# Optimization experiments

Measured on AMD Instinct MI355X. Metric: run time of the kernel, lower is better.

Reference implementation:

```python
import jax, jax.numpy as jnp
import numpy as np

DIM = 128          # per-head dim P (== feature dim of x, y)
HEADS = 8
INNER = DIM * HEADS  # 1024
HIDDEN = int(DIM * 4.0)  # 512
EPS = 1e-5
LS_INIT = 1e-5


def _ln(x, w, b):
    mu = jnp.mean(x, axis=-1, keepdims=True)
    var = jnp.var(x, axis=-1, keepdims=True)
    return (x - mu) * jax.lax.rsqrt(var + EPS) * w + b


def setup_inputs() -> dict:
    key = jax.random.key(0)
    ks = jax.random.split(key, 10)
    B, N, M = 8, 1024, 1024
    s_in = 1.0 / np.sqrt(DIM)
    s_inner = 1.0 / np.sqrt(INNER)
    s_hid = 1.0 / np.sqrt(HIDDEN)
    return {
        "x": jax.random.normal(ks[0], (B, N, DIM), jnp.float32),
        "y": jax.random.normal(ks[1], (B, M, DIM), jnp.float32),
        "norm_x_w": jnp.ones((DIM,), jnp.float32),
        "norm_x_b": jnp.zeros((DIM,), jnp.float32),
        "norm_y_w": jnp.ones((DIM,), jnp.float32),
        "norm_y_b": jnp.zeros((DIM,), jnp.float32),
        "q_w": jax.random.uniform(ks[2], (INNER, DIM), jnp.float32, -s_in, s_in),
        "kv_w": jax.random.uniform(ks[3], (2 * INNER, DIM), jnp.float32, -s_in, s_in),
        "proj_w": jax.random.uniform(ks[4], (DIM, INNER), jnp.float32, -s_inner, s_inner),
        "proj_b": jax.random.uniform(ks[5], (DIM,), jnp.float32, -s_inner, s_inner),
        "ls1_gamma": jnp.full((DIM,), LS_INIT, jnp.float32),
        "norm_out_w": jnp.ones((DIM,), jnp.float32),
        "norm_out_b": jnp.zeros((DIM,), jnp.float32),
        "fc1_w": jax.random.uniform(ks[6], (HIDDEN, DIM), jnp.float32, -s_in, s_in),
        "fc1_b": jax.random.uniform(ks[7], (HIDDEN,), jnp.float32, -s_in, s_in),
        "fc2_w": jax.random.uniform(ks[8], (DIM, HIDDEN), jnp.float32, -s_hid, s_hid),
        "fc2_b": jax.random.uniform(ks[9], (DIM,), jnp.float32, -s_hid, s_hid),
        "ls2_gamma": jnp.full((DIM,), LS_INIT, jnp.float32),
    }


def reference(x, y, norm_x_w, norm_x_b, norm_y_w, norm_y_b, q_w, kv_w,
              proj_w, proj_b, ls1_gamma, norm_out_w, norm_out_b,
              fc1_w, fc1_b, fc2_w, fc2_b, ls2_gamma):
    B, N, P = x.shape
    M = y.shape[1]
    scale = P ** (-0.5)

    xn = _ln(x, norm_x_w, norm_x_b)
    yn = _ln(y, norm_y_w, norm_y_b)

    # q: (B,N,H,P) -> bhnp ; kv: (B,M,2,H,P)
    q = (xn @ q_w.T).reshape(B, N, HEADS, P).transpose(0, 2, 1, 3)
    kv = (yn @ kv_w.T).reshape(B, M, 2, HEADS, P)
    k = kv[:, :, 0].transpose(0, 2, 1, 3)  # bhmp
    v = kv[:, :, 1].transpose(0, 2, 1, 3)  # bhmp

    attn = jnp.einsum('bhnp,bhmp->bhnm', q, k) * scale
    attn = jax.nn.softmax(attn, axis=-1)
    o = jnp.einsum('bhnm,bhmp->bhnp', attn, v)
    o = o.transpose(0, 2, 1, 3).reshape(B, N, INNER)
    o = o @ proj_w.T + proj_b
    x = x + o * ls1_gamma

    h = _ln(x, norm_out_w, norm_out_b)
    h = jax.nn.relu(h @ fc1_w.T + fc1_b)
    h = h @ fc2_w.T + fc2_b
    x = x + h * ls2_gamma
    return x
```

## Files before the change

### kernel.cpp

```cpp
#include <hip/hip_runtime.h>
#include <stdint.h>

#define DIM    128
#define HEADS  8
#define INNER  1024
#define HIDDEN 512
#define BATCH  8
#define SEQ    1024
#define ROWS   8192

typedef __attribute__((ext_vector_type(8))) short bf16x8;
typedef __attribute__((ext_vector_type(4))) float f32x4;
typedef __attribute__((ext_vector_type(4))) unsigned short u16x4;

#define QSCALE (0.08838834764831845f * 1.4426950408889634f)

#define AS1 __attribute__((address_space(1)))
#define AS3 __attribute__((address_space(3)))

static __device__ __forceinline__ float b2f(unsigned short u) {
    union { float f; unsigned int i; } v; v.i = ((unsigned int)u) << 16; return v.f;
}
static __device__ __forceinline__ unsigned short f2b(float f) {
    union { float f; unsigned int i; } v; v.f = f;
    unsigned int x = v.i;
    return (unsigned short)((x + 0x7fffu + ((x >> 16) & 1u)) >> 16);
}
static __device__ __forceinline__ unsigned int cvt_pk_bf16(float a, float b) {
    unsigned int r;
    asm("v_cvt_pk_bf16_f32 %0, %1, %2" : "=v"(r) : "v"(a), "v"(b));
    return r;
}
static __device__ __forceinline__ void gl_lds16(const unsigned short* g, unsigned short* l) {
    __builtin_amdgcn_global_load_lds((AS1 void*)g, (AS3 void*)l, 16, 0, 0);
}

static __device__ __forceinline__ size_t pa_idx(int row, int k, int K) {
    return ((size_t)((row >> 4) * (K >> 5) + (k >> 5)) << 9)
         + (size_t)(((((k >> 3) & 3) << 4) + (row & 15)) << 3) + (size_t)(k & 7);
}

template<int K>
static __device__ __forceinline__ void cvtw(const float* __restrict__ W,
                                            unsigned short* __restrict__ Wp, int j)
{
    const int c  = j & 15;
    const int gw = (j >> 4) & 3;
    const int blk = j >> 6;
    const int ks = blk & ((K >> 5) - 1);
    const int nt = blk / (K >> 5);
    const int n  = nt * 16 + c;
    const int kb = ks * 32 + gw * 8;
    const float4 a = *(const float4*)(W + (size_t)n * K + kb);
    const float4 b = *(const float4*)(W + (size_t)n * K + kb + 4);
    u16x4 o0, o1;
    o0[0] = f2b(a.x); o0[1] = f2b(a.y); o0[2] = f2b(a.z); o0[3] = f2b(a.w);
    o1[0] = f2b(b.x); o1[1] = f2b(b.y); o1[2] = f2b(b.z); o1[3] = f2b(b.w);
    *(u16x4*)(Wp + (size_t)j * 8)     = o0;
    *(u16x4*)(Wp + (size_t)j * 8 + 4) = o1;
}

__global__ __launch_bounds__(256)
void cvt_all_kernel(const float* __restrict__ s0, unsigned short* __restrict__ d0,
                    const float* __restrict__ s1, unsigned short* __restrict__ d1,
                    const float* __restrict__ s2, unsigned short* __restrict__ d2,
                    const float* __restrict__ s3, unsigned short* __restrict__ d3,
                    const float* __restrict__ s4, unsigned short* __restrict__ d4)
{
    int j = blockIdx.x * 256 + threadIdx.x;
    if (j < 16384)                 { cvtw<128>(s0, d0, j);  return; }
    if ((j -= 16384) < 32768)      { cvtw<128>(s1, d1, j);  return; }
    if ((j -= 32768) < 16384)      { cvtw<1024>(s2, d2, j); return; }
    if ((j -= 16384) < 8192)       { cvtw<128>(s3, d3, j);  return; }
    j -= 8192;                       cvtw<512>(s4, d4, j);
}

static __device__ __forceinline__ void ln_row(const float* __restrict__ in,
                                              const float* __restrict__ w,
                                              const float* __restrict__ b,
                                              unsigned short* __restrict__ out,
                                              int row, int lane)
{
    const float2 xv = *(const float2*)(in + (size_t)row*DIM + lane*2);
    float x0 = xv.x, x1 = xv.y;
    float s = x0 + x1;
    float q = x0*x0 + x1*x1;
    #pragma unroll
    for (int off = 32; off > 0; off >>= 1) {
        s += __shfl_xor(s, off);
        q += __shfl_xor(q, off);
    }
    const float mu  = s * (1.0f/128.0f);
    const float var = q * (1.0f/128.0f) - mu*mu;
    const float rs  = rsqrtf(var + 1e-5f);
    const float2 wv = *(const float2*)(w + lane*2);
    const float2 bv = *(const float2*)(b + lane*2);
    unsigned short o0 = f2b((x0 - mu) * rs * wv.x + bv.x);
    unsigned short o1 = f2b((x1 - mu) * rs * wv.y + bv.y);
    *(unsigned int*)(out + pa_idx(row, lane*2, 128)) = (unsigned int)o0 | ((unsigned int)o1 << 16);
}

__global__ __launch_bounds__(256)
void ln_dual_kernel(const float* __restrict__ inx, const float* __restrict__ wx,
                    const float* __restrict__ bx, unsigned short* __restrict__ outx,
                    const float* __restrict__ iny, const float* __restrict__ wy,
                    const float* __restrict__ by, unsigned short* __restrict__ outy)
{
    const int row  = blockIdx.x * 4 + (threadIdx.x >> 6);
    const int lane = threadIdx.x & 63;
    if (blockIdx.y == 0) ln_row(inx, wx, bx, outx, row, lane);
    else                 ln_row(iny, wy, by, outy, row, lane);
}

__global__ __launch_bounds__(256)
void qkv_kernel(const unsigned short* __restrict__ xn,
                const unsigned short* __restrict__ yn,
                const unsigned short* __restrict__ wq,
                const unsigned short* __restrict__ wkv,
                unsigned short* __restrict__ qb,
                unsigned short* __restrict__ kpm,
                unsigned short* __restrict__ vpm)
{
    const int lane = threadIdx.x & 63;
    const int wave = threadIdx.x >> 6;
    const int g    = lane >> 4;
    const int c16  = lane & 15;
    const int bx   = blockIdx.x;
    const bool isq = bx < 16;
    const unsigned short* A = isq ? xn : yn;
    const unsigned short* W = isq ? wq : wkv;
    const int nt0  = (isq ? bx : bx - 16) * 4;
    const int mb   = blockIdx.y * 64 + wave * 16;
    const int nb   = nt0 * 16;
    const int mt   = blockIdx.y * 4 + wave;

    f32x4 acc[4];
    #pragma unroll
    for (int t = 0; t < 4; ++t) acc[t] = (f32x4){0.f, 0.f, 0.f, 0.f};

    #pragma unroll
    for (int ks = 0; ks < 4; ++ks) {
        bf16x8 af = *(const bf16x8*)(A + (((size_t)(mt*4 + ks)) << 9) + lane*8);
        #pragma unroll
        for (int t = 0; t < 4; ++t) {
            bf16x8 wf = *(const bf16x8*)(W + (((size_t)((nt0 + t)*4 + ks)) << 9) + lane*8);
            acc[t] = __builtin_amdgcn_mfma_f32_16x16x32_bf16(af, wf, acc[t], 0, 0, 0);
        }
    }

    #pragma unroll
    for (int t = 0; t < 4; ++t) {
        #pragma unroll
        for (int r = 0; r < 4; ++r) {
            const int row = mb + g*4 + r;
            const int col = nb + t*16 + c16;
            const float v = acc[t][r];
            const int bb = row >> 10, m = row & 1023;
            if (isq) {
                const int hh = col >> 7, p = col & 127;
                qb[(((size_t)(bb*HEADS + hh))*SEQ + m)*DIM + p] = f2b(v * QSCALE);
            } else {
                const int chunk = m >> 5;
                if (col < INNER) {
                    const int hh = col >> 7, p = col & 127;
                    const int sl = (m >> 4) & 1, cl = m & 15;
                    const int ksl = p >> 5, gl = (p >> 3) & 3, el = p & 7;
                    kpm[(size_t)(bb*HEADS + hh)*SEQ*DIM
                        + (size_t)((chunk*8 + sl*4 + ksl)*64 + gl*16 + cl)*8 + el] = f2b(v);
                } else {
                    const int c2 = col - INNER;
                    const int hh = c2 >> 7, p = c2 & 127;
                    const int gl = (m >> 3) & 3, el = m & 7;
                    const int pcl = p >> 4, cl = p & 15;
                    vpm[(size_t)(bb*HEADS + hh)*SEQ*DIM
                        + (size_t)((chunk*8 + pcl)*64 + gl*16 + cl)*8 + el] = f2b(v);
                }
            }
        }
    }
}

__global__ __launch_bounds__(512)
void attn_kernel(const unsigned short* __restrict__ qbuf,
                 const unsigned short* __restrict__ kperm,
                 const unsigned short* __restrict__ vperm,
                 unsigned short* __restrict__ obuf)
{
    __shared__ unsigned short kbuf[2][4096];
    __shared__ unsigned short vbuf[2][4096];
    __shared__ unsigned short pls[8][640];

    const int lane = threadIdx.x & 63;
    const int wave = threadIdx.x >> 6;
    const int g    = lane >> 4;
    const int c16  = lane & 15;

    const int j    = blockIdx.x;
    const int bh   = (j & 7) * 8 + (j >> 6);
    const int nblk = (j >> 3) & 7;
    const int n0   = nblk * 128 + wave * 16;
    const int bb   = bh >> 3, hh = bh & 7;

    const unsigned short* Q  = qbuf  + (size_t)bh * SEQ * DIM;
    const unsigned short* Kb = kperm + (size_t)bh * SEQ * DIM;
    const unsigned short* Vb = vperm + (size_t)bh * SEQ * DIM;

    gl_lds16(Kb + wave*512 + lane*8, &kbuf[0][wave*512]);
    gl_lds16(Vb + wave*512 + lane*8, &vbuf[0][wave*512]);

    bf16x8 qf[4];
    #pragma unroll
    for (int ks = 0; ks < 4; ++ks)
        qf[ks] = *(const bf16x8*)(Q + (size_t)(n0 + c16)*DIM + ks*32 + g*8);

    f32x4 oacc[8];
    #pragma unroll
    for (int pc = 0; pc < 8; ++pc) oacc[pc] = (f32x4){0.f,0.f,0.f,0.f};
    float mi = 8.0f;
    float li0 = 0.f, li1 = 0.f;

    __syncthreads();

    int cur = 0;
    for (int it = 0; it < 32; ++it, cur ^= 1) {
        if (it != 31) {
            const unsigned short* Ks = Kb + (size_t)(it + 1) * 4096;
            const unsigned short* Vs = Vb + (size_t)(it + 1) * 4096;
            gl_lds16(Ks + wave*512 + lane*8, &kbuf[cur ^ 1][wave*512]);
            gl_lds16(Vs + wave*512 + lane*8, &vbuf[cur ^ 1][wave*512]);
        }

        bf16x8 kf[2][4];
        #pragma unroll
        for (int s = 0; s < 2; ++s)
            #pragma unroll
            for (int ks = 0; ks < 4; ++ks)
                kf[s][ks] = *(const bf16x8*)&kbuf[cur][(s*4 + ks)*512 + lane*8];

        f32x4 st[2];
        #pragma unroll
        for (int s = 0; s < 2; ++s) {
            f32x4 a = (f32x4){0.f,0.f,0.f,0.f};
            #pragma unroll
            for (int ks = 0; ks < 4; ++ks)
                a = __builtin_amdgcn_mfma_f32_16x16x32_bf16(kf[s][ks], qf[ks], a, 0, 0, 0);
            st[s] = a;
        }

        bf16x8 vf[8];
        #pragma unroll
        for (int pc = 0; pc < 8; ++pc)
            vf[pc] = *(const bf16x8*)&vbuf[cur][(pc*64 + lane)*8];

        float cmax = st[0][0];
        cmax = fmaxf(cmax, st[0][1]); cmax = fmaxf(cmax, st[0][2]); cmax = fmaxf(cmax, st[0][3]);
        cmax = fmaxf(cmax, st[1][0]); cmax = fmaxf(cmax, st[1][1]);
        cmax = fmaxf(cmax, st[1][2]); cmax = fmaxf(cmax, st[1][3]);

        if (!__all(cmax - mi <= 8.0f)) {
            float rmax = cmax;
            rmax = fmaxf(rmax, __shfl_xor(rmax, 16));
            rmax = fmaxf(rmax, __shfl_xor(rmax, 32));
            const float mnew  = fmaxf(mi, rmax);
            const float alpha = exp2f(mi - mnew);
            mi = mnew;
            li0 *= alpha; li1 *= alpha;
            float ar[4];
            #pragma unroll
            for (int r = 0; r < 4; ++r) ar[r] = __shfl(alpha, g*4 + r);
            #pragma unroll
            for (int pc = 0; pc < 8; ++pc)
                #pragma unroll
                for (int r = 0; r < 4; ++r) oacc[pc][r] *= ar[r];
        }

        uint2 pw[2];
        {
            float p0 = exp2f(st[0][0] - mi), p1 = exp2f(st[0][1] - mi);
            float p2 = exp2f(st[0][2] - mi), p3 = exp2f(st[0][3] - mi);
            float p4 = exp2f(st[1][0] - mi), p5 = exp2f(st[1][1] - mi);
            float p6 = exp2f(st[1][2] - mi), p7 = exp2f(st[1][3] - mi);
            li0 += (p0 + p1) + (p2 + p3);
            li1 += (p4 + p5) + (p6 + p7);
            pw[0].x = cvt_pk_bf16(p0, p1); pw[0].y = cvt_pk_bf16(p2, p3);
            pw[1].x = cvt_pk_bf16(p4, p5); pw[1].y = cvt_pk_bf16(p6, p7);
        }

        unsigned short* pbase = &pls[wave][0];
        *(uint2*)(pbase + c16*40 + 0*16 + g*4) = pw[0];
        *(uint2*)(pbase + c16*40 + 1*16 + g*4) = pw[1];

        bf16x8 pa = *(const bf16x8*)(pbase + c16*40 + g*8);
        #pragma unroll
        for (int pc = 0; pc < 8; ++pc)
            oacc[pc] = __builtin_amdgcn_mfma_f32_16x16x32_bf16(pa, vf[pc], oacc[pc], 0, 0, 0);

        __syncthreads();
    }

    float li = li0 + li1;
    li += __shfl_xor(li, 16);
    li += __shfl_xor(li, 32);
    float lr[4];
    #pragma unroll
    for (int r = 0; r < 4; ++r) lr[r] = 1.f / __shfl(li, g*4 + r);
    #pragma unroll
    for (int pc = 0; pc < 8; ++pc)
        #pragma unroll
        for (int r = 0; r < 4; ++r) {
            const int row = bb*SEQ + n0 + g*4 + r;
            const int k   = hh*DIM + pc*16 + c16;
            obuf[pa_idx(row, k, INNER)] = f2b(oacc[pc][r] * lr[r]);
        }
}

__global__ __launch_bounds__(256)
void projln_kernel(const unsigned short* __restrict__ A,
                   const unsigned short* __restrict__ W,
                   const float* __restrict__ bias,
                   const float* __restrict__ gamma,
                   const float* __restrict__ xres,
                   float* __restrict__ x1,
                   const float* __restrict__ lnw, const float* __restrict__ lnb,
                   unsigned short* __restrict__ hin)
{
    __shared__ float part[4][16][2];

    const int lane = threadIdx.x & 63;
    const int wave = threadIdx.x >> 6;
    const int g    = lane >> 4;
    const int c16  = lane & 15;
    const int mt   = blockIdx.x;

    f32x4 acc[2];
    acc[0] = (f32x4){0.f,0.f,0.f,0.f};
    acc[1] = (f32x4){0.f,0.f,0.f,0.f};

    #pragma unroll 4
    for (int ks = 0; ks < 32; ++ks) {
        bf16x8 af = *(const bf16x8*)(A + (((size_t)(mt*32 + ks)) << 9) + lane*8);
        #pragma unroll
        for (int t = 0; t < 2; ++t) {
            bf16x8 wf = *(const bf16x8*)(W + (((size_t)((wave*2 + t)*32 + ks)) << 9) + lane*8);
            acc[t] = __builtin_amdgcn_mfma_f32_16x16x32_bf16(af, wf, acc[t], 0, 0, 0);
        }
    }

    float v[2][4];
    #pragma unroll
    for (int t = 0; t < 2; ++t) {
        const int col = wave*32 + t*16 + c16;
        const float bb = bias[col], gg = gamma[col];
        #pragma unroll
        for (int r = 0; r < 4; ++r) {
            const int row = mt*16 + g*4 + r;
            const float xv = xres[(size_t)row*DIM + col];
            v[t][r] = xv + (acc[t][r] + bb) * gg;
            x1[(size_t)row*DIM + col] = v[t][r];
        }
    }
    #pragma unroll
    for (int r = 0; r < 4; ++r) {
        float s = v[0][r] + v[1][r];
        float q = v[0][r]*v[0][r] + v[1][r]*v[1][r];
        #pragma unroll
        for (int off = 1; off < 16; off <<= 1) {
            s += __shfl_xor(s, off);
            q += __shfl_xor(q, off);
        }
        if (c16 == 0) { part[wave][g*4+r][0] = s; part[wave][g*4+r][1] = q; }
    }
    __syncthreads();

    #pragma unroll
    for (int r = 0; r < 4; ++r) {
        const int lr = g*4 + r;
        const float s = part[0][lr][0] + part[1][lr][0] + part[2][lr][0] + part[3][lr][0];
        const float q = part[0][lr][1] + part[1][lr][1] + part[2][lr][1] + part[3][lr][1];
        const float mu  = s * (1.0f/128.0f);
        const float var = q * (1.0f/128.0f) - mu*mu;
        const float rs  = rsqrtf(var + 1e-5f);
        const int row = mt*16 + lr;
        #pragma unroll
        for (int t = 0; t < 2; ++t) {
            const int col = wave*32 + t*16 + c16;
            const float hv = (v[t][r] - mu) * rs * lnw[col] + lnb[col];
            hin[pa_idx(row, col, 128)] = f2b(hv);
        }
    }
}

__global__ __launch_bounds__(256)
void fc_kernel(const unsigned short* __restrict__ hin,
               const unsigned short* __restrict__ W1,
               const float* __restrict__ b1,
               const unsigned short* __restrict__ W2,
               const float* __restrict__ b2,
               const float* __restrict__ gamma2,
               const float* __restrict__ x1,
               float* __restrict__ dout)
{
    __shared__ unsigned short h[16][520];

    const int lane = threadIdx.x & 63;
    const int wave = threadIdx.x >> 6;
    const int g    = lane >> 4;
    const int c16  = lane & 15;
    const int mt   = blockIdx.x;

    f32x4 a1[8];
    #pragma unroll
    for (int t = 0; t < 8; ++t) a1[t] = (f32x4){0.f,0.f,0.f,0.f};
    #pragma unroll
    for (int ks = 0; ks < 4; ++ks) {
        bf16x8 af = *(const bf16x8*)(hin + (((size_t)(mt*4 + ks)) << 9) + lane*8);
        #pragma unroll
        for (int t = 0; t < 8; ++t) {
            const int nt = wave*8 + t;
            bf16x8 wf = *(const bf16x8*)(W1 + (((size_t)(nt*4 + ks)) << 9) + lane*8);
            a1[t] = __builtin_amdgcn_mfma_f32_16x16x32_bf16(af, wf, a1[t], 0, 0, 0);
        }
    }
    #pragma unroll
    for (int t = 0; t < 8; ++t) {
        const int col = wave*128 + t*16 + c16;
        const float bb = b1[col];
        #pragma unroll
        for (int r = 0; r < 4; ++r)
            h[g*4 + r][col] = f2b(fmaxf(a1[t][r] + bb, 0.f));
    }
    __syncthreads();

    f32x4 a2[2];
    a2[0] = (f32x4){0.f,0.f,0.f,0.f};
    a2[1] = (f32x4){0.f,0.f,0.f,0.f};
    #pragma unroll 4
    for (int ks = 0; ks < 16; ++ks) {
        bf16x8 af = *(const bf16x8*)&h[c16][ks*32 + g*8];
        #pragma unroll
        for (int t = 0; t < 2; ++t) {
            const int nt = wave*2 + t;
            bf16x8 wf = *(const bf16x8*)(W2 + (((size_t)(nt*16 + ks)) << 9) + lane*8);
            a2[t] = __builtin_amdgcn_mfma_f32_16x16x32_bf16(af, wf, a2[t], 0, 0, 0);
        }
    }
    #pragma unroll
    for (int t = 0; t < 2; ++t) {
        const int col = wave*32 + t*16 + c16;
        const float bb = b2[col], gg = gamma2[col];
        #pragma unroll
        for (int r = 0; r < 4; ++r) {
            const int row = mt*16 + g*4 + r;
            dout[(size_t)row*DIM + col] = x1[(size_t)row*DIM + col] + (a2[t][r] + bb) * gg;
        }
    }
}

extern "C" void kernel_launch(void* const* d_in, const int* in_sizes, int n_in,
                              void* d_out, int out_size, void* d_ws, size_t ws_size,
                              hipStream_t stream)
{
    const float* x         = (const float*)d_in[0];
    const float* y         = (const float*)d_in[1];
    const float* norm_x_w  = (const float*)d_in[2];
    const float* norm_x_b  = (const float*)d_in[3];
    const float* norm_y_w  = (const float*)d_in[4];
    const float* norm_y_b  = (const float*)d_in[5];
    const float* q_w       = (const float*)d_in[6];
    const float* kv_w      = (const float*)d_in[7];
    const float* proj_w    = (const float*)d_in[8];
    const float* proj_b    = (const float*)d_in[9];
    const float* ls1_gamma = (const float*)d_in[10];
    const float* norm_o_w  = (const float*)d_in[11];
    const float* norm_o_b  = (const float*)d_in[12];
    const float* fc1_w     = (const float*)d_in[13];
    const float* fc1_b     = (const float*)d_in[14];
    const float* fc2_w     = (const float*)d_in[15];
    const float* fc2_b     = (const float*)d_in[16];
    const float* ls2_gamma = (const float*)d_in[17];

    char* ws = (char*)d_ws;
    size_t off = 0;
    auto alloc = [&](size_t bytes) {
        void* p = ws + off;
        off += (bytes + 255) & ~(size_t)255;
        return p;
    };
    unsigned short* xn  = (unsigned short*)alloc((size_t)ROWS*DIM*2);
    unsigned short* yn  = (unsigned short*)alloc((size_t)ROWS*DIM*2);
    unsigned short* qb  = (unsigned short*)alloc((size_t)ROWS*INNER*2);
    unsigned short* kpm = (unsigned short*)alloc((size_t)ROWS*INNER*2);
    unsigned short* vpm = (unsigned short*)alloc((size_t)ROWS*INNER*2);
    unsigned short* ob  = (unsigned short*)alloc((size_t)ROWS*INNER*2);
    float*          x1  = (float*)alloc((size_t)ROWS*DIM*4);
    unsigned short* hin = (unsigned short*)alloc((size_t)ROWS*DIM*2);
    unsigned short* wq   = (unsigned short*)alloc((size_t)INNER*DIM*2);
    unsigned short* wkv  = (unsigned short*)alloc((size_t)2*INNER*DIM*2);
    unsigned short* wpr  = (unsigned short*)alloc((size_t)DIM*INNER*2);
    unsigned short* wf1  = (unsigned short*)alloc((size_t)HIDDEN*DIM*2);
    unsigned short* wf2  = (unsigned short*)alloc((size_t)DIM*HIDDEN*2);

    cvt_all_kernel<<<dim3(320), 256, 0, stream>>>(
        q_w, wq, kv_w, wkv, proj_w, wpr, fc1_w, wf1, fc2_w, wf2);

    ln_dual_kernel<<<dim3(ROWS/4, 2), 256, 0, stream>>>(
        x, norm_x_w, norm_x_b, xn, y, norm_y_w, norm_y_b, yn);

    qkv_kernel<<<dim3(48, ROWS/64), 256, 0, stream>>>(xn, yn, wq, wkv, qb, kpm, vpm);

    attn_kernel<<<dim3(512), 512, 0, stream>>>(qb, kpm, vpm, ob);

    projln_kernel<<<dim3(ROWS/16), 256, 0, stream>>>(
        ob, wpr, proj_b, ls1_gamma, x, x1, norm_o_w, norm_o_b, hin);

    fc_kernel<<<dim3(ROWS/16), 256, 0, stream>>>(
        hin, wf1, fc1_b, wf2, fc2_b, ls2_gamma, x1, (float*)d_out);
}
```

Measured before the change: 118.9 us.

## Vectorize QKV epilogue stores and double attention K/V tile per barrier

The QKV projection swaps operand roles for the Q and K blocks, so each lane holds 4 consecutive output features and writes them as one packed 8-byte store instead of scattered 2-byte stores. V blocks keep their original orientation and also pack 4 consecutive sequence positions per store. In attention, each pipeline stage now loads 64 keys instead of 32, which halves the number of block barriers and makes each async load batch larger. The cost is double the LDS for the K/V buffers, which may reduce occupancy.

```diff
diff --git a/kernel.cpp b/kernel.cpp
--- a/kernel.cpp
+++ b/kernel.cpp
@@ -126,56 +126,72 @@
     const int g    = lane >> 4;
     const int c16  = lane & 15;
     const int bx   = blockIdx.x;
-    const bool isq = bx < 16;
-    const unsigned short* A = isq ? xn : yn;
-    const unsigned short* W = isq ? wq : wkv;
-    const int nt0  = (isq ? bx : bx - 16) * 4;
-    const int mb   = blockIdx.y * 64 + wave * 16;
-    const int nb   = nt0 * 16;
-    const int mt   = blockIdx.y * 4 + wave;
+    const int by   = blockIdx.y;
 
     f32x4 acc[4];
     #pragma unroll
     for (int t = 0; t < 4; ++t) acc[t] = (f32x4){0.f, 0.f, 0.f, 0.f};
 
-    #pragma unroll
-    for (int ks = 0; ks < 4; ++ks) {
-        bf16x8 af = *(const bf16x8*)(A + (((size_t)(mt*4 + ks)) << 9) + lane*8);
+    if (bx < 32) {
+        const bool isq = bx < 16;
+        const unsigned short* W = isq ? wq : wkv;
+        const unsigned short* Aact = isq ? xn : yn;
+        const int wt = (bx & 15) * 4 + wave;
+        #pragma unroll
+        for (int ks = 0; ks < 4; ++ks) {
+            bf16x8 wf = *(const bf16x8*)(W + (((size_t)(wt*4 + ks)) << 9) + lane*8);
+            #pragma unroll
+            for (int t = 0; t < 4; ++t) {
+                bf16x8 af = *(const bf16x8*)(Aact + (((size_t)((by*4 + t)*4 + ks)) << 9) + lane*8);
+                acc[t] = __builtin_amdgcn_mfma_f32_16x16x32_bf16(wf, af, acc[t], 0, 0, 0);
+            }
+        }
+        const int n_w0 = (bx & 15)*64 + wave*16 + g*4;
+        const int hh = n_w0 >> 7;
+        const int p0 = n_w0 & 127;
         #pragma unroll
         for (int t = 0; t < 4; ++t) {
-            bf16x8 wf = *(const bf16x8*)(W + (((size_t)((nt0 + t)*4 + ks)) << 9) + lane*8);
-            acc[t] = __builtin_amdgcn_mfma_f32_16x16x32_bf16(af, wf, acc[t], 0, 0, 0);
-        }
-    }
-
-    #pragma unroll
-    for (int t = 0; t < 4; ++t) {
-        #pragma unroll
-        for (int r = 0; r < 4; ++r) {
-            const int row = mb + g*4 + r;
-            const int col = nb + t*16 + c16;
-            const float v = acc[t][r];
-            const int bb = row >> 10, m = row & 1023;
+            const int m_row = by*64 + t*16 + c16;
+            const int bb = m_row >> 10, m = m_row & 1023;
+            u16x4 o;
             if (isq) {
-                const int hh = col >> 7, p = col & 127;
-                qb[(((size_t)(bb*HEADS + hh))*SEQ + m)*DIM + p] = f2b(v * QSCALE);
+                o[0] = f2b(acc[t][0]*QSCALE); o[1] = f2b(acc[t][1]*QSCALE);
+                o[2] = f2b(acc[t][2]*QSCALE); o[3] = f2b(acc[t][3]*QSCALE);
+                *(u16x4*)&qb[(((size_t)(bb*HEADS + hh))*SEQ + m)*DIM + p0] = o;
             } else {
-                const int chunk = m >> 5;
-                if (col < INNER) {
-                    const int hh = col >> 7, p = col & 127;
-                    const int sl = (m >> 4) & 1, cl = m & 15;
-                    const int ksl = p >> 5, gl = (p >> 3) & 3, el = p & 7;
-                    kpm[(size_t)(bb*HEADS + hh)*SEQ*DIM
-                        + (size_t)((chunk*8 + sl*4 + ksl)*64 + gl*16 + cl)*8 + el] = f2b(v);
-                } else {
-                    const int c2 = col - INNER;
-                    const int hh = c2 >> 7, p = c2 & 127;
-                    const int gl = (m >> 3) & 3, el = m & 7;
-                    const int pcl = p >> 4, cl = p & 15;
-                    vpm[(size_t)(bb*HEADS + hh)*SEQ*DIM
-                        + (size_t)((chunk*8 + pcl)*64 + gl*16 + cl)*8 + el] = f2b(v);
-                }
-            }
+                o[0] = f2b(acc[t][0]); o[1] = f2b(acc[t][1]);
+                o[2] = f2b(acc[t][2]); o[3] = f2b(acc[t][3]);
+                const int chunk = m >> 5, sl = (m >> 4) & 1, cl = m & 15;
+                const int ksl = p0 >> 5, gl = (p0 >> 3) & 3, el0 = p0 & 7;
+                *(u16x4*)&kpm[(size_t)(bb*HEADS + hh)*SEQ*DIM
+                    + (size_t)((chunk*8 + sl*4 + ksl)*64 + gl*16 + cl)*8 + el0] = o;
+            }
+        }
+    } else {
+        const int mt = by*4 + wave;
+        #pragma unroll
+        for (int ks = 0; ks < 4; ++ks) {
+            bf16x8 af = *(const bf16x8*)(yn + (((size_t)(mt*4 + ks)) << 9) + lane*8);
+            #pragma unroll
+            for (int t = 0; t < 4; ++t) {
+                const int nt = 64 + (bx - 32)*4 + t;
+                bf16x8 wf = *(const bf16x8*)(wkv + (((size_t)(nt*4 + ks)) << 9) + lane*8);
+                acc[t] = __builtin_amdgcn_mfma_f32_16x16x32_bf16(af, wf, acc[t], 0, 0, 0);
+            }
+        }
+        const int m_row0 = by*64 + wave*16 + g*4;
+        const int bb = m_row0 >> 10;
+        const int m0 = m_row0 & 1023;
+        const int chunk = m0 >> 5, gl = (m0 >> 3) & 3, el0 = m0 & 7;
+        #pragma unroll
+        for (int t = 0; t < 4; ++t) {
+            const int p = (bx - 32)*64 + t*16 + c16;
+            const int hh = p >> 7, pp = p & 127, pcl = pp >> 4, cl = pp & 15;
+            u16x4 o;
+            o[0] = f2b(acc[t][0]); o[1] = f2b(acc[t][1]);
+            o[2] = f2b(acc[t][2]); o[3] = f2b(acc[t][3]);
+            *(u16x4*)&vpm[(size_t)(bb*HEADS + hh)*SEQ*DIM
+                + (size_t)((chunk*8 + pcl)*64 + gl*16 + cl)*8 + el0] = o;
         }
     }
 }
@@ -186,8 +202,8 @@
                  const unsigned short* __restrict__ vperm,
                  unsigned short* __restrict__ obuf)
 {
-    __shared__ unsigned short kbuf[2][4096];
-    __shared__ unsigned short vbuf[2][4096];
+    __shared__ unsigned short kbuf[2][8192];
+    __shared__ unsigned short vbuf[2][8192];
     __shared__ unsigned short pls[8][640];
 
     const int lane = threadIdx.x & 63;
@@ -205,8 +221,11 @@
     const unsigned short* Kb = kperm + (size_t)bh * SEQ * DIM;
     const unsigned short* Vb = vperm + (size_t)bh * SEQ * DIM;
 
-    gl_lds16(Kb + wave*512 + lane*8, &kbuf[0][wave*512]);
-    gl_lds16(Vb + wave*512 + lane*8, &vbuf[0][wave*512]);
+    #pragma unroll
+    for (int i = 0; i < 4; ++i) {
+        gl_lds16(Kb + (wave*4 + i)*512 + lane*8, &kbuf[0][(wave*4 + i)*512]);
+        gl_lds16(Vb + (wave*4 + i)*512 + lane*8, &vbuf[0][(wave*4 + i)*512]);
+    }
 
     bf16x8 qf[4];
     #pragma unroll
@@ -222,78 +241,81 @@
     __syncthreads();
 
     int cur = 0;
-    for (int it = 0; it < 32; ++it, cur ^= 1) {
-        if (it != 31) {
-            const unsigned short* Ks = Kb + (size_t)(it + 1) * 4096;
-            const unsigned short* Vs = Vb + (size_t)(it + 1) * 4096;
-            gl_lds16(Ks + wave*512 + lane*8, &kbuf[cur ^ 1][wave*512]);
-            gl_lds16(Vs + wave*512 + lane*8, &vbuf[cur ^ 1][wave*512]);
-        }
-
-        bf16x8 kf[2][4];
-        #pragma unroll
-        for (int s = 0; s < 2; ++s)
+    for (int ip = 0; ip < 16; ++ip, cur ^= 1) {
+        if (ip != 15) {
+            const unsigned short* Ks = Kb + (size_t)(ip + 1) * 8192;
+            const unsigned short* Vs = Vb + (size_t)(ip + 1) * 8192;
             #pragma unroll
-            for (int ks = 0; ks < 4; ++ks)
-                kf[s][ks] = *(const bf16x8*)&kbuf[cur][(s*4 + ks)*512 + lane*8];
-
-        f32x4 st[2];
-        #pragma unroll
-        for (int s = 0; s < 2; ++s) {
-            f32x4 a = (f32x4){0.f,0.f,0.f,0.f};
+            for (int i = 0; i < 4; ++i) {
+                gl_lds16(Ks + (wave*4 + i)*512 + lane*8, &kbuf[cur ^ 1][(wave*4 + i)*512]);
+                gl_lds16(Vs + (wave*4 + i)*512 + lane*8, &vbuf[cur ^ 1][(wave*4 + i)*512]);
+            }
+        }
+
+        f32x4 st[4];
+        #pragma unroll
+        for (int c = 0; c < 2; ++c)
             #pragma unroll
-            for (int ks = 0; ks < 4; ++ks)
-                a = __builtin_amdgcn_mfma_f32_16x16x32_bf16(kf[s][ks], qf[ks], a, 0, 0, 0);
-            st[s] = a;
-        }
-
-        bf16x8 vf[8];
-        #pragma unroll
-        for (int pc = 0; pc < 8; ++pc)
-            vf[pc] = *(const bf16x8*)&vbuf[cur][(pc*64 + lane)*8];
-
-        float cmax = st[0][0];
-        cmax = fmaxf(cmax, st[0][1]); cmax = fmaxf(cmax, st[0][2]); cmax = fmaxf(cmax, st[0][3]);
-        cmax = fmaxf(cmax, st[1][0]); cmax = fmaxf(cmax, st[1][1]);
-        cmax = fmaxf(cmax, st[1][2]); cmax = fmaxf(cmax, st[1][3]);
-
-        if (!__all(cmax - mi <= 8.0f)) {
-            float rmax = cmax;
-            rmax = fmaxf(rmax, __shfl_xor(rmax, 16));
-            rmax = fmaxf(rmax, __shfl_xor(rmax, 32));
-            const float mnew  = fmaxf(mi, rmax);
-            const float alpha = exp2f(mi - mnew);
-            mi = mnew;
-            li0 *= alpha; li1 *= alpha;
-            float ar[4];
-            #pragma unroll
-            for (int r = 0; r < 4; ++r) ar[r] = __shfl(alpha, g*4 + r);
+            for (int s = 0; s < 2; ++s) {
+                f32x4 a = (f32x4){0.f,0.f,0.f,0.f};
+                #pragma unroll
+                for (int ks = 0; ks < 4; ++ks) {
+                    bf16x8 kf = *(const bf16x8*)&kbuf[cur][c*4096 + (s*4 + ks)*512 + lane*8];
+                    a = __builtin_amdgcn_mfma_f32_16x16x32_bf16(kf, qf[ks], a, 0, 0, 0);
+                }
+                st[c*2 + s] = a;
+            }
+
+        #pragma unroll
+        for (int c = 0; c < 2; ++c) {
+            bf16x8 vf[8];
             #pragma unroll
             for (int pc = 0; pc < 8; ++pc)
+                vf[pc] = *(const bf16x8*)&vbuf[cur][c*4096 + (pc*64 + lane)*8];
+
+            const f32x4 sa = st[c*2 + 0];
+            const f32x4 sb = st[c*2 + 1];
+            float cmax = fmaxf(fmaxf(fmaxf(sa[0], sa[1]), fmaxf(sa[2], sa[3])),
+                               fmaxf(fmaxf(sb[0], sb[1]), fmaxf(sb[2], sb[3])));
+
+            if (!__all(cmax - mi <= 8.0f)) {
+                float rmax = cmax;
+                rmax = fmaxf(rmax, __shfl_xor(rmax, 16));
+                rmax = fmaxf(rmax, __shfl_xor(rmax, 32));
+                const float mnew  = fmaxf(mi, rmax);
+                const float alpha = exp2f(mi - mnew);
+                mi = mnew;
+                li0 *= alpha; li1 *= alpha;
+                float ar[4];
                 #pragma unroll
-                for (int r = 0; r < 4; ++r) oacc[pc][r] *= ar[r];
-        }
-
-        uint2 pw[2];
-        {
-            float p0 = exp2f(st[0][0] - mi), p1 = exp2f(st[0][1] - mi);
-            float p2 = exp2f(st[0][2] - mi), p3 = exp2f(st[0][3] - mi);
-            float p4 = exp2f(st[1][0] - mi), p5 = exp2f(st[1][1] - mi);
-            float p6 = exp2f(st[1][2] - mi), p7 = exp2f(st[1][3] - mi);
-            li0 += (p0 + p1) + (p2 + p3);
-            li1 += (p4 + p5) + (p6 + p7);
-            pw[0].x = cvt_pk_bf16(p0, p1); pw[0].y = cvt_pk_bf16(p2, p3);
-            pw[1].x = cvt_pk_bf16(p4, p5); pw[1].y = cvt_pk_bf16(p6, p7);
-        }
-
-        unsigned short* pbase = &pls[wave][0];
-        *(uint2*)(pbase + c16*40 + 0*16 + g*4) = pw[0];
-        *(uint2*)(pbase + c16*40 + 1*16 + g*4) = pw[1];
-
-        bf16x8 pa = *(const bf16x8*)(pbase + c16*40 + g*8);
-        #pragma unroll
-        for (int pc = 0; pc < 8; ++pc)
-            oacc[pc] = __builtin_amdgcn_mfma_f32_16x16x32_bf16(pa, vf[pc], oacc[pc], 0, 0, 0);
+                for (int r = 0; r < 4; ++r) ar[r] = __shfl(alpha, g*4 + r);
+                #pragma unroll
+                for (int pc = 0; pc < 8; ++pc)
+                    #pragma unroll
+                    for (int r = 0; r < 4; ++r) oacc[pc][r] *= ar[r];
+            }
+
+            uint2 pw[2];
+            {
+                float p0 = exp2f(sa[0] - mi), p1 = exp2f(sa[1] - mi);
+                float p2 = exp2f(sa[2] - mi), p3 = exp2f(sa[3] - mi);
+                float p4 = exp2f(sb[0] - mi), p5 = exp2f(sb[1] - mi);
+                float p6 = exp2f(sb[2] - mi), p7 = exp2f(sb[3] - mi);
+                li0 += (p0 + p1) + (p2 + p3);
+                li1 += (p4 + p5) + (p6 + p7);
+                pw[0].x = cvt_pk_bf16(p0, p1); pw[0].y = cvt_pk_bf16(p2, p3);
+                pw[1].x = cvt_pk_bf16(p4, p5); pw[1].y = cvt_pk_bf16(p6, p7);
+            }
+
+            unsigned short* pbase = &pls[wave][0];
+            *(uint2*)(pbase + c16*40 + 0*16 + g*4) = pw[0];
+            *(uint2*)(pbase + c16*40 + 1*16 + g*4) = pw[1];
+
+            bf16x8 pa = *(const bf16x8*)(pbase + c16*40 + g*8);
+            #pragma unroll
+            for (int pc = 0; pc < 8; ++pc)
+                oacc[pc] = __builtin_amdgcn_mfma_f32_16x16x32_bf16(pa, vf[pc], oacc[pc], 0, 0, 0);
+        }
 
         __syncthreads();
     }
```

Result: faster. 112.6 us (-5.3%).
